# Optimization experiments

Hardware: AMD Instinct MI355X
Metric: run time of the kernel (lower is better)

## Reference

```python
import jax, jax.numpy as jnp
import numpy as np

B, H, SQ, SK, D, DV = 2, 16, 2048, 2048, 64, 64
SCALE_FACTOR = 2.0   # non-standard: applied AFTER softmax as 1/scale_factor
DROPOUT_P = 0.1
DROPOUT_KEY = 42     # fixed key -> deterministic dropout mask


def setup_inputs() -> dict:
    key = jax.random.key(0)
    kq, kk, kv = jax.random.split(key, 3)
    return {
        "query": jax.random.normal(kq, (B, H, SQ, D), dtype=jnp.float32),
        "k": jax.random.normal(kk, (H, SK, D), dtype=jnp.float32),
        "v": jax.random.normal(kv, (H, SK, DV), dtype=jnp.float32),
    }


def reference(query, k, v):
    # qk = query @ k^T : [B,H,Sq,Sk]
    qk = jnp.einsum("bhqd,hkd->bhqk", query, k)
    inv_scale = 1.0 / SCALE_FACTOR
    probs = jax.nn.softmax(qk, axis=-1) * inv_scale
    # dropout (train mode, inverted-dropout scaling), deterministic mask
    keep = jax.random.bernoulli(jax.random.key(DROPOUT_KEY), 1.0 - DROPOUT_P, probs.shape)
    probs = jnp.where(keep, probs / (1.0 - DROPOUT_P), 0.0)
    # output = probs @ v : [B,H,Sq,Dv]
    return jnp.einsum("bhqk,hkv->bhqv", probs, v)
```

## Files before the change

### kernel.cpp

```cpp
#include <hip/hip_runtime.h>
#include <stdint.h>
#include <math.h>

namespace {
constexpr int Bb = 2, Hh = 16, SQc = 2048, SKc = 2048, Dc = 64, DVc = 64;
constexpr int TK = 64;
constexpr float LOG2E = 1.4426950408889634f;
constexpr uint64_t KEEP_T = 0xE666666666667000ull;

typedef __attribute__((ext_vector_type(8))) short short8;
typedef __attribute__((ext_vector_type(4))) float f32x4;

__device__ __forceinline__ uint32_t rotl_(uint32_t x, int r) {
  return __builtin_amdgcn_alignbit(x, x, 32 - r);
}

__device__ __forceinline__ uint64_t tf_bits64(uint32_t ctr) {
  const uint32_t KS1 = 42u, KS2 = 0x1BD11BF0u;
  uint32_t x0, x1;
  x1 = ctr + KS1;
  x0 = x1;        x1 = rotl_(x1, 13); x1 ^= x0;
  x0 += x1;       x1 = rotl_(x1, 15); x1 ^= x0;
  x0 += x1;       x1 = rotl_(x1, 26); x1 ^= x0;
  x0 += x1;       x1 = rotl_(x1,  6); x1 ^= x0;
  x1 += KS2 + 1u;
  x0 += KS1 + x1; x1 = rotl_(x1, 17); x1 ^= x0;
  x0 += x1;       x1 = rotl_(x1, 29); x1 ^= x0;
  x0 += x1;       x1 = rotl_(x1, 16); x1 ^= x0;
  x0 += x1;       x1 = rotl_(x1, 24); x1 ^= x0;
  x1 += 2u;
  x0 += KS2 + x1; x1 = rotl_(x1, 13); x1 ^= x0;
  x0 += x1;       x1 = rotl_(x1, 15); x1 ^= x0;
  x0 += x1;       x1 = rotl_(x1, 26); x1 ^= x0;
  x0 += x1;       x1 = rotl_(x1,  6); x1 ^= x0;
  x1 += KS1 + 3u;
  x0 += x1;       x1 = rotl_(x1, 17); x1 ^= x0;
  x0 += x1;       x1 = rotl_(x1, 29); x1 ^= x0;
  x0 += x1;       x1 = rotl_(x1, 16); x1 ^= x0;
  x0 += x1;       x1 = rotl_(x1, 24); x1 ^= x0;
  x1 += KS2 + 4u;
  x0 += KS1 + x1; x1 = rotl_(x1, 13); x1 ^= x0;
  x0 += x1;       x1 = rotl_(x1, 15); x1 ^= x0;
  x0 += x1;       x1 = rotl_(x1, 26); x1 ^= x0;
  x0 += x1;       x1 = rotl_(x1,  6); x1 ^= x0;
  return ((uint64_t)(x0 + KS2) << 32) | (uint64_t)(x1 + 5u);
}

__device__ __forceinline__ uint32_t f2bf_u(float x) {
  uint32_t u = __float_as_uint(x);
  u += 0x7FFFu + ((u >> 16) & 1u);
  return u >> 16;
}

__device__ __forceinline__ void gl_lds16(const void* g, void* l) {
  __builtin_amdgcn_global_load_lds(
      (const __attribute__((address_space(1))) unsigned int*)g,
      (__attribute__((address_space(3))) unsigned int*)l, 16, 0, 0);
}
}

__global__ __launch_bounds__(256) void prep_kernel(
    const float* __restrict__ k, const float* __restrict__ v,
    unsigned short* __restrict__ Khg, unsigned short* __restrict__ Klg,
    unsigned short* __restrict__ Vtg) {
  __shared__ float Vs[64 * 65];
  const int t = threadIdx.x;
  const int h = blockIdx.x >> 5;
  const int kt = blockIdx.x & 31;
  const size_t src = ((size_t)h * SKc + kt * 64) * Dc;
  const size_t tb = (size_t)(h * 32 + kt) * 4096;
#pragma unroll
  for (int i = 0; i < 4; ++i) {
    int idx = t + 256 * i;
    int row = idx >> 4, d0 = (idx & 15) << 2;
    float4 kv = *(const float4*)(k + src + row * Dc + d0);
    uint32_t hx = f2bf_u(kv.x), hy = f2bf_u(kv.y), hz = f2bf_u(kv.z), hw = f2bf_u(kv.w);
    uint32_t lx = f2bf_u(kv.x - __uint_as_float(hx << 16));
    uint32_t ly = f2bf_u(kv.y - __uint_as_float(hy << 16));
    uint32_t lz = f2bf_u(kv.z - __uint_as_float(hz << 16));
    uint32_t lw = f2bf_u(kv.w - __uint_as_float(hw << 16));
    int phys = row * 64 + (((d0 >> 3) ^ (row & 7)) << 3) + (d0 & 7);
    *(ushort4*)(Khg + tb + phys) =
        make_ushort4((unsigned short)hx, (unsigned short)hy, (unsigned short)hz, (unsigned short)hw);
    *(ushort4*)(Klg + tb + phys) =
        make_ushort4((unsigned short)lx, (unsigned short)ly, (unsigned short)lz, (unsigned short)lw);
    float4 vv = *(const float4*)(v + src + row * Dc + d0);
    *(float4*)(&Vs[row * 65 + d0]) = vv;
  }
  __syncthreads();
  const int dv = t >> 2;
  const int j0 = (t & 3) << 1;
#pragma unroll
  for (int g = 0; g < 2; ++g) {
    int chunk = j0 + g;
    unsigned short tmp[8];
#pragma unroll
    for (int s = 0; s < 8; ++s)
      tmp[s] = (unsigned short)f2bf_u(Vs[(chunk * 8 + s) * 65 + dv]);
    *(short8*)(Vtg + tb + dv * 64 + ((chunk ^ (dv & 7)) << 3)) = *(const short8*)tmp;
  }
}

__global__ __launch_bounds__(512, 4) void attn_main(
    const float* __restrict__ q, const unsigned short* __restrict__ Khg,
    const unsigned short* __restrict__ Klg, const unsigned short* __restrict__ Vtg,
    float* __restrict__ out) {
  __shared__ __align__(16) unsigned short stag[2][12288];

  const int t = threadIdx.x;
  const int lane = t & 63;
  const int w = t >> 6;
  const int lm = lane & 15;
  const int quad = lane >> 4;

  const int vid = (blockIdx.x & 7) * 64 + (blockIdx.x >> 3);
  const int qt = vid & 15;
  const int h = (vid >> 4) & 15;
  const int b = vid >> 8;
  const int qrow = qt * 128 + w * 16 + lm;

  short8 qh[2], ql[2];
  {
    const float* qp = q + (((size_t)(b * Hh + h)) * SQc + qrow) * Dc;
#pragma unroll
    for (int c = 0; c < 2; ++c) {
#pragma unroll
      for (int j2 = 0; j2 < 2; ++j2) {
        float4 x = *(const float4*)(qp + c * 32 + quad * 8 + j2 * 4);
        float xs[4] = {x.x * LOG2E, x.y * LOG2E, x.z * LOG2E, x.w * LOG2E};
#pragma unroll
        for (int j = 0; j < 4; ++j) {
          uint32_t hb = f2bf_u(xs[j]);
          float lo = xs[j] - __uint_as_float(hb << 16);
          qh[c][j2 * 4 + j] = (short)hb;
          ql[c][j2 * 4 + j] = (short)f2bf_u(lo);
        }
      }
    }
  }

  const char* kh_t = (const char*)Khg + (size_t)(h * 32) * 8192;
  const char* kl_t = (const char*)Klg + (size_t)(h * 32) * 8192;
  const char* vt_t = (const char*)Vtg + (size_t)(h * 32) * 8192;

  f32x4 acc[4] = {{0.f, 0.f, 0.f, 0.f}, {0.f, 0.f, 0.f, 0.f},
                  {0.f, 0.f, 0.f, 0.f}, {0.f, 0.f, 0.f, 0.f}};
  float l_i = 0.f;

  const int e = lm & 7;
  const int a0s = lm * 64 + ((quad ^ e) << 3);
  const int a1s = lm * 64 + (((quad + 4) ^ e) << 3);

  const int pa0 = ((quad & 1) * 32 + lm) << 2;
  const int pa1 = pa0 + 64;
  const uint32_t sel = (quad >= 2) ? 0x07060302u : 0x05040100u;

  uint32_t ctile = ((uint32_t)((b * Hh + h) * SQc + qrow)) * (uint32_t)SKc +
                   (uint32_t)(quad * 4);

  const int soff = w * 1024 + lane * 16;

  {
    char* db = (char*)&stag[0][0];
    gl_lds16(kh_t + soff, db + soff);
    gl_lds16(kl_t + soff, db + 8192 + soff);
    gl_lds16(vt_t + soff, db + 16384 + soff);
  }

#pragma unroll 1
  for (int i = 0; i < 32; ++i, ctile += TK) {
    __syncthreads();
    if (i < 31) {
      const size_t tile = (size_t)(i + 1) * 8192;
      char* db = (char*)&stag[(i & 1) ^ 1][0];
      gl_lds16(kh_t + tile + soff, db + soff);
      gl_lds16(kl_t + tile + soff, db + 8192 + soff);
      gl_lds16(vt_t + tile + soff, db + 16384 + soff);
    }
    const unsigned short* sb = &stag[i & 1][0];

#pragma unroll
    for (int c = 0; c < 2; ++c) {
      f32x4 s0 = {0.f, 0.f, 0.f, 0.f}, s1 = {0.f, 0.f, 0.f, 0.f};
#pragma unroll
      for (int d = 0; d < 2; ++d) {
        const int ad = (d == 0) ? a0s : a1s;
        short8 kh0 = *(const short8*)&sb[ad + (2 * c) * 1024];
        short8 kl0 = *(const short8*)&sb[ad + (2 * c) * 1024 + 4096];
        s0 = __builtin_amdgcn_mfma_f32_16x16x32_bf16(kh0, qh[d], s0, 0, 0, 0);
        s0 = __builtin_amdgcn_mfma_f32_16x16x32_bf16(kl0, qh[d], s0, 0, 0, 0);
        s0 = __builtin_amdgcn_mfma_f32_16x16x32_bf16(kh0, ql[d], s0, 0, 0, 0);
        short8 kh1 = *(const short8*)&sb[ad + (2 * c + 1) * 1024];
        short8 kl1 = *(const short8*)&sb[ad + (2 * c + 1) * 1024 + 4096];
        s1 = __builtin_amdgcn_mfma_f32_16x16x32_bf16(kh1, qh[d], s1, 0, 0, 0);
        s1 = __builtin_amdgcn_mfma_f32_16x16x32_bf16(kl1, qh[d], s1, 0, 0, 0);
        s1 = __builtin_amdgcn_mfma_f32_16x16x32_bf16(kh1, ql[d], s1, 0, 0, 0);
      }

      uint32_t pkc[4];
#pragma unroll
      for (int r = 0; r < 4; ++r) {
        float p0 = __builtin_amdgcn_exp2f(s0[r]);
        float p1 = __builtin_amdgcn_exp2f(s1[r]);
        l_i += p0 + p1;
        uint64_t b0 = tf_bits64(ctile + (uint32_t)(c * 32 + r));
        uint64_t b1 = tf_bits64(ctile + (uint32_t)(c * 32 + 16 + r));
        float k0 = (b0 < KEEP_T) ? p0 : 0.0f;
        float k1 = (b1 < KEEP_T) ? p1 : 0.0f;
        uint32_t pk;
        asm("v_cvt_pk_bf16_f32 %0, %1, %2" : "=v"(pk) : "v"(k0), "v"(k1));
        pkc[r] = pk;
      }

      short8 pb;
      {
        uint32_t e0 = (uint32_t)__builtin_amdgcn_ds_bpermute(pa0, (int)pkc[0]);
        uint32_t e1 = (uint32_t)__builtin_amdgcn_ds_bpermute(pa0, (int)pkc[1]);
        uint32_t e2 = (uint32_t)__builtin_amdgcn_ds_bpermute(pa0, (int)pkc[2]);
        uint32_t e3 = (uint32_t)__builtin_amdgcn_ds_bpermute(pa0, (int)pkc[3]);
        uint32_t f0 = (uint32_t)__builtin_amdgcn_ds_bpermute(pa1, (int)pkc[0]);
        uint32_t f1 = (uint32_t)__builtin_amdgcn_ds_bpermute(pa1, (int)pkc[1]);
        uint32_t f2 = (uint32_t)__builtin_amdgcn_ds_bpermute(pa1, (int)pkc[2]);
        uint32_t f3 = (uint32_t)__builtin_amdgcn_ds_bpermute(pa1, (int)pkc[3]);
        uint32_t w0 = __builtin_amdgcn_perm(e1, e0, sel);
        uint32_t w1 = __builtin_amdgcn_perm(e3, e2, sel);
        uint32_t w2 = __builtin_amdgcn_perm(f1, f0, sel);
        uint32_t w3 = __builtin_amdgcn_perm(f3, f2, sel);
        uint32_t tmp[4] = {w0, w1, w2, w3};
        pb = *(const short8*)tmp;
      }

      {
        const int ac = (c == 0) ? a0s : a1s;
#pragma unroll
        for (int nb = 0; nb < 4; ++nb) {
          short8 vb = *(const short8*)&sb[ac + nb * 1024 + 8192];
          acc[nb] = __builtin_amdgcn_mfma_f32_16x16x32_bf16(vb, pb, acc[nb], 0, 0, 0);
        }
      }
    }
  }

  l_i += __shfl_xor(l_i, 16);
  l_i += __shfl_xor(l_i, 32);
  const float sc = (0.5f / 0.9f) / l_i;
  float* op = out + (((size_t)(b * Hh + h)) * SQc + qrow) * DVc;
#pragma unroll
  for (int nb = 0; nb < 4; ++nb) {
    float4 o = make_float4(acc[nb][0] * sc, acc[nb][1] * sc,
                           acc[nb][2] * sc, acc[nb][3] * sc);
    *(float4*)(op + nb * 16 + quad * 4) = o;
  }
}

extern "C" void kernel_launch(void* const* d_in, const int* in_sizes, int n_in,
                              void* d_out, int out_size, void* d_ws, size_t ws_size,
                              hipStream_t stream) {
  const float* q = (const float*)d_in[0];
  const float* k = (const float*)d_in[1];
  const float* v = (const float*)d_in[2];
  float* out = (float*)d_out;
  unsigned short* Khg = (unsigned short*)d_ws;
  unsigned short* Klg = Khg + (size_t)Hh * SKc * Dc;
  unsigned short* Vtg = Klg + (size_t)Hh * SKc * Dc;
  prep_kernel<<<dim3(Hh * 32), 256, 0, stream>>>(k, v, Khg, Klg, Vtg);
  attn_main<<<dim3(Bb * Hh * (SQc / 128)), 512, 0, stream>>>(q, Khg, Klg, Vtg, out);
}
```

Baseline: 358.4 us.

## Precompute dropout keep-mask as a bitmask in a separate kernel

Adds a mask_kernel that evaluates the Threefry dropout RNG for every (row, key) element and packs the keep decisions into 64-bit ballot words in workspace. The attention kernel then loads one 64-bit word per row per key tile and tests bits instead of running two 20-round hash computations per score element inside the MFMA loop. The goal is to take heavy integer ALU work off the critical attention path, where it competes with the exp and MFMA work. The cost is an extra launch, about 16 MB of mask writes and reads through memory, and a larger workspace requirement.

```diff
diff --git a/kernel.cpp b/kernel.cpp
--- a/kernel.cpp
+++ b/kernel.cpp
@@ -59,6 +59,20 @@
 }
 }
 
+__global__ __launch_bounds__(256, 8) void mask_kernel(
+    unsigned long long* __restrict__ Mg) {
+  const int lane = threadIdx.x & 63;
+  const uint32_t wv = blockIdx.x * 4u + (threadIdx.x >> 6);
+  uint32_t ctr = wv * (256u * 64u) + (uint32_t)lane;
+  unsigned long long* op = Mg + (size_t)wv * 256;
+#pragma unroll 2
+  for (int j = 0; j < 256; ++j) {
+    uint64_t bits = tf_bits64(ctr + (uint32_t)(j * 64));
+    unsigned long long m = __ballot(bits < KEEP_T);
+    if (lane == 0) op[j] = m;
+  }
+}
+
 __global__ __launch_bounds__(256) void prep_kernel(
     const float* __restrict__ k, const float* __restrict__ v,
     unsigned short* __restrict__ Khg, unsigned short* __restrict__ Klg,
@@ -104,7 +118,7 @@
 __global__ __launch_bounds__(512, 4) void attn_main(
     const float* __restrict__ q, const unsigned short* __restrict__ Khg,
     const unsigned short* __restrict__ Klg, const unsigned short* __restrict__ Vtg,
-    float* __restrict__ out) {
+    const unsigned long long* __restrict__ Mg, float* __restrict__ out) {
   __shared__ __align__(16) unsigned short stag[2][12288];
 
   const int t = threadIdx.x;
@@ -118,6 +132,7 @@
   const int h = (vid >> 4) & 15;
   const int b = vid >> 8;
   const int qrow = qt * 128 + w * 16 + lm;
+  const uint32_t mrow = (uint32_t)((b * Hh + h) * SQc + qrow);
 
   short8 qh[2], ql[2];
   {
@@ -155,9 +170,6 @@
   const int pa1 = pa0 + 64;
   const uint32_t sel = (quad >= 2) ? 0x07060302u : 0x05040100u;
 
-  uint32_t ctile = ((uint32_t)((b * Hh + h) * SQc + qrow)) * (uint32_t)SKc +
-                   (uint32_t)(quad * 4);
-
   const int soff = w * 1024 + lane * 16;
 
   {
@@ -168,7 +180,8 @@
   }
 
 #pragma unroll 1
-  for (int i = 0; i < 32; ++i, ctile += TK) {
+  for (int i = 0; i < 32; ++i) {
+    const uint2 mw = *(const uint2*)&Mg[(size_t)mrow * 32 + i];
     __syncthreads();
     if (i < 31) {
       const size_t tile = (size_t)(i + 1) * 8192;
@@ -197,16 +210,15 @@
         s1 = __builtin_amdgcn_mfma_f32_16x16x32_bf16(kh1, ql[d], s1, 0, 0, 0);
       }
 
+      const uint32_t ms = ((c == 0) ? mw.x : mw.y) >> (quad * 4);
       uint32_t pkc[4];
 #pragma unroll
       for (int r = 0; r < 4; ++r) {
         float p0 = __builtin_amdgcn_exp2f(s0[r]);
         float p1 = __builtin_amdgcn_exp2f(s1[r]);
         l_i += p0 + p1;
-        uint64_t b0 = tf_bits64(ctile + (uint32_t)(c * 32 + r));
-        uint64_t b1 = tf_bits64(ctile + (uint32_t)(c * 32 + 16 + r));
-        float k0 = (b0 < KEEP_T) ? p0 : 0.0f;
-        float k1 = (b1 < KEEP_T) ? p1 : 0.0f;
+        float k0 = (ms & (1u << r)) ? p0 : 0.0f;
+        float k1 = (ms & (1u << (r + 16))) ? p1 : 0.0f;
         uint32_t pk;
         asm("v_cvt_pk_bf16_f32 %0, %1, %2" : "=v"(pk) : "v"(k0), "v"(k1));
         pkc[r] = pk;
@@ -263,6 +275,8 @@
   unsigned short* Khg = (unsigned short*)d_ws;
   unsigned short* Klg = Khg + (size_t)Hh * SKc * Dc;
   unsigned short* Vtg = Klg + (size_t)Hh * SKc * Dc;
+  unsigned long long* Mg = (unsigned long long*)(Vtg + (size_t)Hh * SKc * Dc);
   prep_kernel<<<dim3(Hh * 32), 256, 0, stream>>>(k, v, Khg, Klg, Vtg);
-  attn_main<<<dim3(Bb * Hh * (SQc / 128)), 512, 0, stream>>>(q, Khg, Klg, Vtg, out);
-}
+  mask_kernel<<<dim3(2048), 256, 0, stream>>>(Mg);
+  attn_main<<<dim3(Bb * Hh * (SQc / 128)), 512, 0, stream>>>(q, Khg, Klg, Vtg, Mg, out);
+}
```

Measured after the change: 461.7 us. +28.8%, slower.

## Specialize waves: producer waves generate dropout masks, consumer waves compute attention

Applied to the files above, without the earlier changes.

Half the waves in each block become producers. They run the Threefry generator and write 64-bit keep-mask words for the next key tile into double-buffered shared memory. The other four waves each process two 16-row query groups and read the packed mask bits instead of computing the hash inline. The goal is to take the heavy integer PRNG work off the MFMA/exp critical path and overlap it with the matrix math. In exchange, the compute waves hold twice the accumulators and Q fragments, which raises register pressure, and the PRNG throughput now depends on only four waves.

```diff
diff --git a/kernel.cpp b/kernel.cpp
--- a/kernel.cpp
+++ b/kernel.cpp
@@ -46,6 +46,20 @@
   return ((uint64_t)(x0 + KS2) << 32) | (uint64_t)(x1 + 5u);
 }
 
+__device__ __forceinline__ uint32_t tf_word32(uint32_t cb) {
+  uint32_t m = 0u;
+#pragma unroll
+  for (int j = 0; j < 32; j += 4) {
+    uint64_t b0 = tf_bits64(cb + (uint32_t)j);
+    uint64_t b1 = tf_bits64(cb + (uint32_t)j + 1u);
+    uint64_t b2 = tf_bits64(cb + (uint32_t)j + 2u);
+    uint64_t b3 = tf_bits64(cb + (uint32_t)j + 3u);
+    m |= (b0 < KEEP_T ? (1u << j) : 0u) | (b1 < KEEP_T ? (2u << j) : 0u) |
+         (b2 < KEEP_T ? (4u << j) : 0u) | (b3 < KEEP_T ? (8u << j) : 0u);
+  }
+  return m;
+}
+
 __device__ __forceinline__ uint32_t f2bf_u(float x) {
   uint32_t u = __float_as_uint(x);
   u += 0x7FFFu + ((u >> 16) & 1u);
@@ -106,6 +120,7 @@
     const unsigned short* __restrict__ Klg, const unsigned short* __restrict__ Vtg,
     float* __restrict__ out) {
   __shared__ __align__(16) unsigned short stag[2][12288];
+  __shared__ unsigned long long maskb[2][128];
 
   const int t = threadIdx.x;
   const int lane = t & 63;
@@ -117,11 +132,38 @@
   const int qt = vid & 15;
   const int h = (vid >> 4) & 15;
   const int b = vid >> 8;
-  const int qrow = qt * 128 + w * 16 + lm;
-
-  short8 qh[2], ql[2];
-  {
-    const float* qp = q + (((size_t)(b * Hh + h)) * SQc + qrow) * Dc;
+
+  const char* kh_t = (const char*)Khg + (size_t)(h * 32) * 8192;
+  const char* kl_t = (const char*)Klg + (size_t)(h * 32) * 8192;
+  const char* vt_t = (const char*)Vtg + (size_t)(h * 32) * 8192;
+
+  if (w >= 4) {
+    const int p = w - 4;
+    const int rp = p * 32 + (lane & 31);
+    const int half = lane >> 5;
+    const uint32_t grow = (uint32_t)((b * Hh + h) * SQc + qt * 128 + rp);
+    const uint32_t cb0 = grow * (uint32_t)SKc + (uint32_t)(half * 32);
+    uint32_t* mp0 = (uint32_t*)&maskb[0][rp] + half;
+    uint32_t* mp1 = (uint32_t*)&maskb[1][rp] + half;
+    *mp0 = tf_word32(cb0);
+#pragma unroll 1
+    for (int i = 0; i < 32; ++i) {
+      __syncthreads();
+      if (i < 31) {
+        uint32_t m = tf_word32(cb0 + (uint32_t)((i + 1) * TK));
+        *(((i + 1) & 1) ? mp1 : mp0) = m;
+      }
+    }
+    return;
+  }
+
+  const int cw = w;
+  const int qb = qt * 128 + cw * 32;
+
+  short8 qh[2][2], ql[2][2];
+#pragma unroll
+  for (int g = 0; g < 2; ++g) {
+    const float* qp = q + (((size_t)(b * Hh + h)) * SQc + qb + g * 16 + lm) * Dc;
 #pragma unroll
     for (int c = 0; c < 2; ++c) {
 #pragma unroll
@@ -132,20 +174,15 @@
         for (int j = 0; j < 4; ++j) {
           uint32_t hb = f2bf_u(xs[j]);
           float lo = xs[j] - __uint_as_float(hb << 16);
-          qh[c][j2 * 4 + j] = (short)hb;
-          ql[c][j2 * 4 + j] = (short)f2bf_u(lo);
+          qh[g][c][j2 * 4 + j] = (short)hb;
+          ql[g][c][j2 * 4 + j] = (short)f2bf_u(lo);
         }
       }
     }
   }
 
-  const char* kh_t = (const char*)Khg + (size_t)(h * 32) * 8192;
-  const char* kl_t = (const char*)Klg + (size_t)(h * 32) * 8192;
-  const char* vt_t = (const char*)Vtg + (size_t)(h * 32) * 8192;
-
-  f32x4 acc[4] = {{0.f, 0.f, 0.f, 0.f}, {0.f, 0.f, 0.f, 0.f},
-                  {0.f, 0.f, 0.f, 0.f}, {0.f, 0.f, 0.f, 0.f}};
-  float l_i = 0.f;
+  f32x4 acc[2][4] = {};
+  float l_i[2] = {0.f, 0.f};
 
   const int e = lm & 7;
   const int a0s = lm * 64 + ((quad ^ e) << 3);
@@ -155,101 +192,112 @@
   const int pa1 = pa0 + 64;
   const uint32_t sel = (quad >= 2) ? 0x07060302u : 0x05040100u;
 
-  uint32_t ctile = ((uint32_t)((b * Hh + h) * SQc + qrow)) * (uint32_t)SKc +
-                   (uint32_t)(quad * 4);
-
-  const int soff = w * 1024 + lane * 16;
+  const int soff = cw * 2048 + lane * 16;
 
   {
     char* db = (char*)&stag[0][0];
     gl_lds16(kh_t + soff, db + soff);
+    gl_lds16(kh_t + soff + 1024, db + soff + 1024);
     gl_lds16(kl_t + soff, db + 8192 + soff);
+    gl_lds16(kl_t + soff + 1024, db + 8192 + soff + 1024);
     gl_lds16(vt_t + soff, db + 16384 + soff);
+    gl_lds16(vt_t + soff + 1024, db + 16384 + soff + 1024);
   }
 
 #pragma unroll 1
-  for (int i = 0; i < 32; ++i, ctile += TK) {
+  for (int i = 0; i < 32; ++i) {
     __syncthreads();
     if (i < 31) {
       const size_t tile = (size_t)(i + 1) * 8192;
       char* db = (char*)&stag[(i & 1) ^ 1][0];
       gl_lds16(kh_t + tile + soff, db + soff);
+      gl_lds16(kh_t + tile + soff + 1024, db + soff + 1024);
       gl_lds16(kl_t + tile + soff, db + 8192 + soff);
+      gl_lds16(kl_t + tile + soff + 1024, db + 8192 + soff + 1024);
       gl_lds16(vt_t + tile + soff, db + 16384 + soff);
+      gl_lds16(vt_t + tile + soff + 1024, db + 16384 + soff + 1024);
     }
     const unsigned short* sb = &stag[i & 1][0];
 
 #pragma unroll
-    for (int c = 0; c < 2; ++c) {
-      f32x4 s0 = {0.f, 0.f, 0.f, 0.f}, s1 = {0.f, 0.f, 0.f, 0.f};
-#pragma unroll
-      for (int d = 0; d < 2; ++d) {
-        const int ad = (d == 0) ? a0s : a1s;
-        short8 kh0 = *(const short8*)&sb[ad + (2 * c) * 1024];
-        short8 kl0 = *(const short8*)&sb[ad + (2 * c) * 1024 + 4096];
-        s0 = __builtin_amdgcn_mfma_f32_16x16x32_bf16(kh0, qh[d], s0, 0, 0, 0);
-        s0 = __builtin_amdgcn_mfma_f32_16x16x32_bf16(kl0, qh[d], s0, 0, 0, 0);
-        s0 = __builtin_amdgcn_mfma_f32_16x16x32_bf16(kh0, ql[d], s0, 0, 0, 0);
-        short8 kh1 = *(const short8*)&sb[ad + (2 * c + 1) * 1024];
-        short8 kl1 = *(const short8*)&sb[ad + (2 * c + 1) * 1024 + 4096];
-        s1 = __builtin_amdgcn_mfma_f32_16x16x32_bf16(kh1, qh[d], s1, 0, 0, 0);
-        s1 = __builtin_amdgcn_mfma_f32_16x16x32_bf16(kl1, qh[d], s1, 0, 0, 0);
-        s1 = __builtin_amdgcn_mfma_f32_16x16x32_bf16(kh1, ql[d], s1, 0, 0, 0);
+    for (int g = 0; g < 2; ++g) {
+      const uint64_t w64 = maskb[i & 1][cw * 32 + g * 16 + lm];
+
+#pragma unroll
+      for (int c = 0; c < 2; ++c) {
+        f32x4 s0 = {0.f, 0.f, 0.f, 0.f}, s1 = {0.f, 0.f, 0.f, 0.f};
+#pragma unroll
+        for (int d = 0; d < 2; ++d) {
+          const int ad = (d == 0) ? a0s : a1s;
+          short8 kh0 = *(const short8*)&sb[ad + (2 * c) * 1024];
+          short8 kl0 = *(const short8*)&sb[ad + (2 * c) * 1024 + 4096];
+          s0 = __builtin_amdgcn_mfma_f32_16x16x32_bf16(kh0, qh[g][d], s0, 0, 0, 0);
+          s0 = __builtin_amdgcn_mfma_f32_16x16x32_bf16(kl0, qh[g][d], s0, 0, 0, 0);
+          s0 = __builtin_amdgcn_mfma_f32_16x16x32_bf16(kh0, ql[g][d], s0, 0, 0, 0);
+          short8 kh1 = *(const short8*)&sb[ad + (2 * c + 1) * 1024];
+          short8 kl1 = *(const short8*)&sb[ad + (2 * c + 1) * 1024 + 4096];
+          s1 = __builtin_amdgcn_mfma_f32_16x16x32_bf16(kh1, qh[g][d], s1, 0, 0, 0);
+          s1 = __builtin_amdgcn_mfma_f32_16x16x32_bf16(kl1, qh[g][d], s1, 0, 0, 0);
+          s1 = __builtin_amdgcn_mfma_f32_16x16x32_bf16(kh1, ql[g][d], s1, 0, 0, 0);
+        }
+
+        const uint32_t ms = ((uint32_t)(w64 >> (c * 32))) >> (quad * 4);
+        uint32_t pkc[4];
+#pragma unroll
+        for (int r = 0; r < 4; ++r) {
+          float p0 = __builtin_amdgcn_exp2f(s0[r]);
+          float p1 = __builtin_amdgcn_exp2f(s1[r]);
+          l_i[g] += p0 + p1;
+          float k0 = (ms & (1u << r)) ? p0 : 0.0f;
+          float k1 = (ms & (1u << (16 + r))) ? p1 : 0.0f;
+          uint32_t pk;
+          asm("v_cvt_pk_bf16_f32 %0, %1, %2" : "=v"(pk) : "v"(k0), "v"(k1));
+          pkc[r] = pk;
+        }
+
+        short8 pb;
+        {
+          uint32_t e0 = (uint32_t)__builtin_amdgcn_ds_bpermute(pa0, (int)pkc[0]);
+          uint32_t e1 = (uint32_t)__builtin_amdgcn_ds_bpermute(pa0, (int)pkc[1]);
+          uint32_t e2 = (uint32_t)__builtin_amdgcn_ds_bpermute(pa0, (int)pkc[2]);
+          uint32_t e3 = (uint32_t)__builtin_amdgcn_ds_bpermute(pa0, (int)pkc[3]);
+          uint32_t f0 = (uint32_t)__builtin_amdgcn_ds_bpermute(pa1, (int)pkc[0]);
+          uint32_t f1 = (uint32_t)__builtin_amdgcn_ds_bpermute(pa1, (int)pkc[1]);
+          uint32_t f2 = (uint32_t)__builtin_amdgcn_ds_bpermute(pa1, (int)pkc[2]);
+          uint32_t f3 = (uint32_t)__builtin_amdgcn_ds_bpermute(pa1, (int)pkc[3]);
+          uint32_t w0 = __builtin_amdgcn_perm(e1, e0, sel);
+          uint32_t w1 = __builtin_amdgcn_perm(e3, e2, sel);
+          uint32_t w2 = __builtin_amdgcn_perm(f1, f0, sel);
+          uint32_t w3 = __builtin_amdgcn_perm(f3, f2, sel);
+          uint32_t tmp[4] = {w0, w1, w2, w3};
+          pb = *(const short8*)tmp;
+        }
+
+        {
+          const int ac = (c == 0) ? a0s : a1s;
+#pragma unroll
+          for (int nb = 0; nb < 4; ++nb) {
+            short8 vb = *(const short8*)&sb[ac + nb * 1024 + 8192];
+            acc[g][nb] = __builtin_amdgcn_mfma_f32_16x16x32_bf16(vb, pb, acc[g][nb], 0, 0, 0);
+          }
+        }
       }
-
-      uint32_t pkc[4];
-#pragma unroll
-      for (int r = 0; r < 4; ++r) {
-        float p0 = __builtin_amdgcn_exp2f(s0[r]);
-        float p1 = __builtin_amdgcn_exp2f(s1[r]);
-        l_i += p0 + p1;
-        uint64_t b0 = tf_bits64(ctile + (uint32_t)(c * 32 + r));
-        uint64_t b1 = tf_bits64(ctile + (uint32_t)(c * 32 + 16 + r));
-        float k0 = (b0 < KEEP_T) ? p0 : 0.0f;
-        float k1 = (b1 < KEEP_T) ? p1 : 0.0f;
-        uint32_t pk;
-        asm("v_cvt_pk_bf16_f32 %0, %1, %2" : "=v"(pk) : "v"(k0), "v"(k1));
-        pkc[r] = pk;
-      }
-
-      short8 pb;
-      {
-        uint32_t e0 = (uint32_t)__builtin_amdgcn_ds_bpermute(pa0, (int)pkc[0]);
-        uint32_t e1 = (uint32_t)__builtin_amdgcn_ds_bpermute(pa0, (int)pkc[1]);
-        uint32_t e2 = (uint32_t)__builtin_amdgcn_ds_bpermute(pa0, (int)pkc[2]);
-        uint32_t e3 = (uint32_t)__builtin_amdgcn_ds_bpermute(pa0, (int)pkc[3]);
-        uint32_t f0 = (uint32_t)__builtin_amdgcn_ds_bpermute(pa1, (int)pkc[0]);
-        uint32_t f1 = (uint32_t)__builtin_amdgcn_ds_bpermute(pa1, (int)pkc[1]);
-        uint32_t f2 = (uint32_t)__builtin_amdgcn_ds_bpermute(pa1, (int)pkc[2]);
-        uint32_t f3 = (uint32_t)__builtin_amdgcn_ds_bpermute(pa1, (int)pkc[3]);
-        uint32_t w0 = __builtin_amdgcn_perm(e1, e0, sel);
-        uint32_t w1 = __builtin_amdgcn_perm(e3, e2, sel);
-        uint32_t w2 = __builtin_amdgcn_perm(f1, f0, sel);
-        uint32_t w3 = __builtin_amdgcn_perm(f3, f2, sel);
-        uint32_t tmp[4] = {w0, w1, w2, w3};
-        pb = *(const short8*)tmp;
-      }
-
-      {
-        const int ac = (c == 0) ? a0s : a1s;
-#pragma unroll
-        for (int nb = 0; nb < 4; ++nb) {
-          short8 vb = *(const short8*)&sb[ac + nb * 1024 + 8192];
-          acc[nb] = __builtin_amdgcn_mfma_f32_16x16x32_bf16(vb, pb, acc[nb], 0, 0, 0);
-        }
-      }
-    }
-  }
-
-  l_i += __shfl_xor(l_i, 16);
-  l_i += __shfl_xor(l_i, 32);
-  const float sc = (0.5f / 0.9f) / l_i;
-  float* op = out + (((size_t)(b * Hh + h)) * SQc + qrow) * DVc;
-#pragma unroll
-  for (int nb = 0; nb < 4; ++nb) {
-    float4 o = make_float4(acc[nb][0] * sc, acc[nb][1] * sc,
-                           acc[nb][2] * sc, acc[nb][3] * sc);
-    *(float4*)(op + nb * 16 + quad * 4) = o;
+    }
+  }
+
+#pragma unroll
+  for (int g = 0; g < 2; ++g) {
+    float lg = l_i[g];
+    lg += __shfl_xor(lg, 16);
+    lg += __shfl_xor(lg, 32);
+    const float sc = (0.5f / 0.9f) / lg;
+    float* op = out + (((size_t)(b * Hh + h)) * SQc + qb + g * 16 + lm) * DVc;
+#pragma unroll
+    for (int nb = 0; nb < 4; ++nb) {
+      float4 o = make_float4(acc[g][nb][0] * sc, acc[g][nb][1] * sc,
+                             acc[g][nb][2] * sc, acc[g][nb][3] * sc);
+      *(float4*)(op + nb * 16 + quad * 4) = o;
+    }
   }
 }
 
```

After: 365.5 us. No clear change (+2.0%).
